# Performance work log

Measured on AMD Instinct MI355X. Metric: run time of the kernel, lower is better.

## Reference

```python
import jax, jax.numpy as jnp
import numpy as np

EPS = 1e-8


def setup_inputs() -> dict:
    key = jax.random.key(0)
    kx, kw = jax.random.split(key)
    B, T, D_IN, D_OUT = 2, 2048, 4096, 16384
    x = jax.random.normal(kx, (B, T, D_IN), dtype=jnp.float32)
    # kaiming-uniform-ish scale for a (D_OUT, D_IN) linear weight
    bound = float(np.sqrt(6.0 / D_IN))
    weight = jax.random.uniform(kw, (D_OUT, D_IN), dtype=jnp.float32,
                                minval=-bound, maxval=bound)
    return {"x": x, "weight": weight}


def reference(x, weight):
    # --- ternary weight quantization (STE; value identical in train/eval) ---
    scale_w = jnp.mean(jnp.abs(weight))                       # scalar absmean
    w_q = jnp.clip(jnp.round(weight / (scale_w + EPS)), -1.0, 1.0) * scale_w
    w_quant = weight + jax.lax.stop_gradient(w_q - weight)    # STE

    # --- per-token INT8 activation quantization ---
    gamma = jnp.max(jnp.abs(x), axis=-1, keepdims=True)       # (B, T, 1)
    x_quant = jnp.clip(jnp.round(127.0 * x / (gamma + EPS)), -128.0, 127.0)
    scale_x = gamma / 127.0                                   # (B, T, 1)

    # --- GEMM + dequant epilogue ---
    out = jnp.einsum("btd,od->bto", x_quant, w_quant)         # (B, T, D_OUT)
    return out * scale_x
```

## Files before the change

### kernel.cpp

```cpp
#include <hip/hip_runtime.h>


#define M_ROWS 4096
#define K_DIM  4096
#define N_DIM  16384
#define W_ELEMS (N_DIM * K_DIM)
#define EPSF 1e-8f

using i32x4 = __attribute__((ext_vector_type(4))) int;


__global__ void k_abs_partial(const float4* __restrict__ w4,
                              double* __restrict__ part) {
    const int tid = threadIdx.x;
    int idx = blockIdx.x * 256 + tid;
    double s = 0.0;
    #pragma unroll 4
    for (int it = 0; it < 32; ++it) {
        float4 v = w4[idx + it * (2048 * 256)];
        s += (double)fabsf(v.x) + (double)fabsf(v.y)
           + (double)fabsf(v.z) + (double)fabsf(v.w);
    }
    __shared__ double red[256];
    red[tid] = s;
    __syncthreads();
    for (int o = 128; o > 0; o >>= 1) {
        if (tid < o) red[tid] += red[tid + o];
        __syncthreads();
    }
    if (tid == 0) part[blockIdx.x] = red[0];
}

__global__ void k_abs_final(const double* __restrict__ part,
                            float* __restrict__ scales) {
    const int tid = threadIdx.x;
    double s = 0.0;
    #pragma unroll
    for (int k = 0; k < 8; ++k) s += part[tid + k * 256];
    __shared__ double red[256];
    red[tid] = s;
    __syncthreads();
    for (int o = 128; o > 0; o >>= 1) {
        if (tid < o) red[tid] += red[tid + o];
        __syncthreads();
    }
    if (tid == 0) {
        float sw = (float)(red[0] / (double)W_ELEMS);
        scales[0] = sw;
        scales[1] = sw + EPSF;
    }
}

__global__ void k_wquant(const float4* __restrict__ w4,
                         const float* __restrict__ scales,
                         char4* __restrict__ wq4) {
    const float seps = scales[1];
    int idx = blockIdx.x * 256 + threadIdx.x;
    const int stride = 8192 * 256;
    #pragma unroll
    for (int it = 0; it < 8; ++it) {
        int i = idx + it * stride;
        float4 v = w4[i];
        char4 q;
        q.x = (signed char)(int)fminf(fmaxf(rintf(v.x / seps), -1.0f), 1.0f);
        q.y = (signed char)(int)fminf(fmaxf(rintf(v.y / seps), -1.0f), 1.0f);
        q.z = (signed char)(int)fminf(fmaxf(rintf(v.z / seps), -1.0f), 1.0f);
        q.w = (signed char)(int)fminf(fmaxf(rintf(v.w / seps), -1.0f), 1.0f);
        wq4[i] = q;
    }
}

__global__ void k_xquant(const float4* __restrict__ x4,
                         char4* __restrict__ xq4,
                         float* __restrict__ sx) {
    const int row = blockIdx.x, tid = threadIdx.x;
    const float4* xr = x4 + (size_t)row * (K_DIM / 4);
    float4 v[4];
    float m = 0.0f;
    #pragma unroll
    for (int j = 0; j < 4; ++j) {
        v[j] = xr[tid + j * 256];
        m = fmaxf(m, fmaxf(fmaxf(fabsf(v[j].x), fabsf(v[j].y)),
                           fmaxf(fabsf(v[j].z), fabsf(v[j].w))));
    }
    __shared__ float red[256];
    red[tid] = m;
    __syncthreads();
    for (int o = 128; o > 0; o >>= 1) {
        if (tid < o) red[tid] = fmaxf(red[tid], red[tid + o]);
        __syncthreads();
    }
    const float gamma = red[0];
    const float ge = gamma + EPSF;
    char4* out = xq4 + (size_t)row * (K_DIM / 4);
    #pragma unroll
    for (int j = 0; j < 4; ++j) {
        char4 q;
        q.x = (signed char)(int)fminf(fmaxf(rintf(127.0f * v[j].x / ge), -128.0f), 127.0f);
        q.y = (signed char)(int)fminf(fmaxf(rintf(127.0f * v[j].y / ge), -128.0f), 127.0f);
        q.z = (signed char)(int)fminf(fmaxf(rintf(127.0f * v[j].z / ge), -128.0f), 127.0f);
        q.w = (signed char)(int)fminf(fmaxf(rintf(127.0f * v[j].w / ge), -128.0f), 127.0f);
        out[tid + j * 256] = q;
    }
    if (tid == 0) sx[row] = gamma / 127.0f;
}

__device__ __forceinline__ void gload16(const signed char* g, signed char* l) {
    __builtin_amdgcn_global_load_lds(
        (const __attribute__((address_space(1))) void*)g,
        (__attribute__((address_space(3))) void*)l, 16, 0, 0);
}

#define BAR()   __builtin_amdgcn_s_barrier()
#define LGKM0() asm volatile("s_waitcnt lgkmcnt(0)" ::: "memory")
#define VM6()   asm volatile("s_waitcnt vmcnt(6)" ::: "memory")
#define PRIO1() __builtin_amdgcn_s_setprio(1)
#define PRIO0() __builtin_amdgcn_s_setprio(0)

__global__ __launch_bounds__(512, 2)
void k_gemm8(const signed char* __restrict__ Aq,
             const signed char* __restrict__ Bq,
             const float* __restrict__ sx,
             const float* __restrict__ scales,
             float* __restrict__ C) {
    __shared__ __align__(16) signed char lds[131072];

    const int tid  = threadIdx.x;
    const int lane = tid & 63;
    const int wid  = tid >> 6;
    const int l15  = lane & 15;
    const int qg   = lane >> 4;
    const int swz  = l15 & 7;

    const int bid = blockIdx.x;
    const int wg  = (bid & 7) * 128 + (bid >> 3);
    const int gidx   = wg >> 9;
    const int within = wg & 511;
    const int pm = gidx * 8 + (within & 7);
    const int pn = within >> 3;

    const int wm = (wid >> 2) * 128;
    const int wn = (wid & 3) * 64;

    const int l3 = lane >> 3, l7 = lane & 7;
    const int lane_off = l3 * K_DIM + ((l7 ^ l3) << 4);
    const signed char* Asrc = Aq + (size_t)(pm * 256) * K_DIM + lane_off;
    const signed char* Bsrc = Bq + (size_t)(pn * 256) * K_DIM + lane_off;
    const int ar0 = wid * 8;
    const int br0 = (wid >> 2) * 64 + (wid & 3) * 8;

    auto stageA = [&](int buf, int mh, int kt) {
        const int r0 = mh * 64 + ar0;
        const signed char* s = Asrc + (size_t)r0 * K_DIM + kt * 128;
        signed char* d = lds + buf * 65536 + r0 * 128;
        gload16(s, d);
        gload16(s + (size_t)128 * K_DIM, d + 128 * 128);
    };
    auto stageB = [&](int buf, int nh, int kt) {
        const int r0 = nh * 32 + br0;
        const signed char* s = Bsrc + (size_t)r0 * K_DIM + kt * 128;
        signed char* d = lds + buf * 65536 + 32768 + r0 * 128;
        gload16(s, d);
        gload16(s + (size_t)128 * K_DIM, d + 128 * 128);
    };

    i32x4 acc[8][4];
    #pragma unroll
    for (int a = 0; a < 8; ++a)
        #pragma unroll
        for (int b = 0; b < 4; ++b)
            acc[a][b] = (i32x4){0, 0, 0, 0};

    i32x4 af[8], bf[4];
    auto ldA = [&](int buf, int mh) {
        const signed char* base = lds + buf * 65536;
        #pragma unroll
        for (int fm = 0; fm < 4; ++fm) {
            const int ro = (wm + mh * 64 + fm * 16 + l15) * 128;
            #pragma unroll
            for (int ks = 0; ks < 2; ++ks)
                af[fm * 2 + ks] = *(const i32x4*)(base + ro + (((ks * 4 + qg) ^ swz) << 4));
        }
    };
    auto ldB = [&](int buf, int nh) {
        const signed char* base = lds + buf * 65536 + 32768;
        #pragma unroll
        for (int fn = 0; fn < 2; ++fn) {
            const int ro = (wn + nh * 32 + fn * 16 + l15) * 128;
            #pragma unroll
            for (int ks = 0; ks < 2; ++ks)
                bf[fn * 2 + ks] = *(const i32x4*)(base + ro + (((ks * 4 + qg) ^ swz) << 4));
        }
    };
    auto mma = [&](int mh, int nh) {
        #pragma unroll
        for (int ks = 0; ks < 2; ++ks)
            #pragma unroll
            for (int fm = 0; fm < 4; ++fm)
                #pragma unroll
                for (int fn = 0; fn < 2; ++fn)
                    acc[mh * 4 + fm][nh * 2 + fn] = __builtin_amdgcn_mfma_i32_16x16x64_i8(
                        af[fm * 2 + ks], bf[fn * 2 + ks], acc[mh * 4 + fm][nh * 2 + fn], 0, 0, 0);
    };

    stageA(0, 0, 0); stageB(0, 1, 0); stageA(0, 1, 0); stageB(0, 0, 0);
    stageA(1, 0, 1); stageB(1, 1, 1); stageA(1, 1, 1);
    VM6();
    BAR();

    for (int t = 0; t < 16; ++t) {
        const int k1 = 2 * t + 1;
        const int k2 = (2 * t + 2) & 31;
        const int k3 = (2 * t + 3) & 31;

        ldA(0, 0); ldB(0, 0); stageB(1, 0, k1);
        BAR(); LGKM0(); PRIO1(); mma(0, 0); PRIO0(); BAR();
        ldB(0, 1); stageA(0, 0, k2);
        BAR(); LGKM0(); PRIO1(); mma(0, 1); PRIO0(); BAR();
        ldA(0, 1); stageB(0, 1, k2);
        BAR(); LGKM0(); PRIO1(); mma(1, 1); PRIO0(); BAR();
        ldB(0, 0); stageA(0, 1, k2);
        BAR(); LGKM0(); PRIO1(); mma(1, 0); PRIO0();
        VM6();
        BAR();
        ldA(1, 0); ldB(1, 0); stageB(0, 0, k2);
        BAR(); LGKM0(); PRIO1(); mma(0, 0); PRIO0(); BAR();
        ldB(1, 1); stageA(1, 0, k3);
        BAR(); LGKM0(); PRIO1(); mma(0, 1); PRIO0(); BAR();
        ldA(1, 1); stageB(1, 1, k3);
        BAR(); LGKM0(); PRIO1(); mma(1, 1); PRIO0(); BAR();
        ldB(1, 0); stageA(1, 1, k3);
        BAR(); LGKM0(); PRIO1(); mma(1, 0); PRIO0();
        VM6();
        BAR();
    }
    asm volatile("s_waitcnt vmcnt(0)" ::: "memory");

    const float sw = scales[0];
    const int gn0 = pn * 256 + wn + l15;
    const int rb  = (lane >> 4) * 4;
    #pragma unroll
    for (int mi = 0; mi < 8; ++mi) {
        const int rowoff = (mi >> 2) * 64 + (mi & 3) * 16;
        #pragma unroll
        for (int r = 0; r < 4; ++r) {
            const int gm = pm * 256 + wm + rowoff + rb + r;
            const float s = sx[gm] * sw;
            float* crow = C + (size_t)gm * N_DIM + gn0;
            #pragma unroll
            for (int ni = 0; ni < 4; ++ni)
                crow[(ni >> 1) * 32 + (ni & 1) * 16] = (float)acc[mi][ni][r] * s;
        }
    }
}

extern "C" void kernel_launch(void* const* d_in, const int* in_sizes, int n_in,
                              void* d_out, int out_size, void* d_ws, size_t ws_size,
                              hipStream_t stream) {
    const float* x = (const float*)d_in[0];
    const float* w = (const float*)d_in[1];
    float* out = (float*)d_out;
    char* ws = (char*)d_ws;

    float*  scales = (float*)(ws);
    double* part   = (double*)(ws + 1024);
    float*  sx     = (float*)(ws + 32 * 1024);
    signed char* xq = (signed char*)(ws + 64 * 1024);
    signed char* wq = xq + (size_t)M_ROWS * K_DIM;

    k_abs_partial<<<2048, 256, 0, stream>>>((const float4*)w, part);
    k_abs_final<<<1, 256, 0, stream>>>(part, scales);
    k_wquant<<<8192, 256, 0, stream>>>((const float4*)w, scales, (char4*)wq);
    k_xquant<<<M_ROWS, 256, 0, stream>>>((const float4*)x, (char4*)xq, sx);
    k_gemm8<<<(M_ROWS / 256) * (N_DIM / 256), 512, 0, stream>>>(xq, wq, sx, scales, out);
}
```

Baseline: 402.9 us.

## Double-buffer A/B register fragments and reorder LDS staging in GEMM main loop

Splits the A and B register fragments into two sets each, so all fragments for a k-tile are loaded from LDS in the first two phases and reused across the four MFMA quadrants. Global-to-LDS staging is reordered to match (B before A, a different staging order across phases). This cuts redundant LDS reads (B for nh=0 and A for mh=1 are no longer reloaded) and leaves two phases without LDS reads. It costs extra VGPRs, which may reduce occupancy or cause spills, and the changed staging order must stay consistent with the buffer hazards guarded by VM6 and the barriers.

```diff
diff --git a/kernel.cpp b/kernel.cpp
--- a/kernel.cpp
+++ b/kernel.cpp
@@ -8,7 +8,6 @@
 #define EPSF 1e-8f
 
 using i32x4 = __attribute__((ext_vector_type(4))) int;
-
 
 __global__ void k_abs_partial(const float4* __restrict__ w4,
                               double* __restrict__ part) {
@@ -171,8 +170,8 @@
         for (int b = 0; b < 4; ++b)
             acc[a][b] = (i32x4){0, 0, 0, 0};
 
-    i32x4 af[8], bf[4];
-    auto ldA = [&](int buf, int mh) {
+    i32x4 af0[8], af1[8], bf0[4], bf1[4];
+    auto ldA = [&](i32x4* af, int buf, int mh) {
         const signed char* base = lds + buf * 65536;
         #pragma unroll
         for (int fm = 0; fm < 4; ++fm) {
@@ -182,7 +181,7 @@
                 af[fm * 2 + ks] = *(const i32x4*)(base + ro + (((ks * 4 + qg) ^ swz) << 4));
         }
     };
-    auto ldB = [&](int buf, int nh) {
+    auto ldB = [&](i32x4* bf, int buf, int nh) {
         const signed char* base = lds + buf * 65536 + 32768;
         #pragma unroll
         for (int fn = 0; fn < 2; ++fn) {
@@ -192,7 +191,7 @@
                 bf[fn * 2 + ks] = *(const i32x4*)(base + ro + (((ks * 4 + qg) ^ swz) << 4));
         }
     };
-    auto mma = [&](int mh, int nh) {
+    auto mma = [&](const i32x4* af, const i32x4* bf, int mh, int nh) {
         #pragma unroll
         for (int ks = 0; ks < 2; ++ks)
             #pragma unroll
@@ -203,8 +202,8 @@
                         af[fm * 2 + ks], bf[fn * 2 + ks], acc[mh * 4 + fm][nh * 2 + fn], 0, 0, 0);
     };
 
-    stageA(0, 0, 0); stageB(0, 1, 0); stageA(0, 1, 0); stageB(0, 0, 0);
-    stageA(1, 0, 1); stageB(1, 1, 1); stageA(1, 1, 1);
+    stageB(0, 0, 0); stageB(0, 1, 0); stageA(0, 0, 0); stageA(0, 1, 0);
+    stageB(1, 0, 1); stageB(1, 1, 1); stageA(1, 0, 1);
     VM6();
     BAR();
 
@@ -213,24 +212,24 @@
         const int k2 = (2 * t + 2) & 31;
         const int k3 = (2 * t + 3) & 31;
 
-        ldA(0, 0); ldB(0, 0); stageB(1, 0, k1);
-        BAR(); LGKM0(); PRIO1(); mma(0, 0); PRIO0(); BAR();
-        ldB(0, 1); stageA(0, 0, k2);
-        BAR(); LGKM0(); PRIO1(); mma(0, 1); PRIO0(); BAR();
-        ldA(0, 1); stageB(0, 1, k2);
-        BAR(); LGKM0(); PRIO1(); mma(1, 1); PRIO0(); BAR();
-        ldB(0, 0); stageA(0, 1, k2);
-        BAR(); LGKM0(); PRIO1(); mma(1, 0); PRIO0();
+        ldB(bf0, 0, 0); ldA(af0, 0, 0); stageA(1, 1, k1);
+        BAR(); LGKM0(); PRIO1(); mma(af0, bf0, 0, 0); PRIO0(); BAR();
+        ldB(bf1, 0, 1); ldA(af1, 0, 1); stageB(0, 0, k2);
+        BAR(); LGKM0(); PRIO1(); mma(af0, bf1, 0, 1); PRIO0(); BAR();
+        stageB(0, 1, k2);
+        BAR(); LGKM0(); PRIO1(); mma(af1, bf1, 1, 1); PRIO0(); BAR();
+        stageA(0, 0, k2);
+        BAR(); LGKM0(); PRIO1(); mma(af1, bf0, 1, 0); PRIO0();
         VM6();
         BAR();
-        ldA(1, 0); ldB(1, 0); stageB(0, 0, k2);
-        BAR(); LGKM0(); PRIO1(); mma(0, 0); PRIO0(); BAR();
-        ldB(1, 1); stageA(1, 0, k3);
-        BAR(); LGKM0(); PRIO1(); mma(0, 1); PRIO0(); BAR();
-        ldA(1, 1); stageB(1, 1, k3);
-        BAR(); LGKM0(); PRIO1(); mma(1, 1); PRIO0(); BAR();
-        ldB(1, 0); stageA(1, 1, k3);
-        BAR(); LGKM0(); PRIO1(); mma(1, 0); PRIO0();
+        ldB(bf0, 1, 0); ldA(af0, 1, 0); stageA(0, 1, k2);
+        BAR(); LGKM0(); PRIO1(); mma(af0, bf0, 0, 0); PRIO0(); BAR();
+        ldB(bf1, 1, 1); ldA(af1, 1, 1); stageB(1, 0, k3);
+        BAR(); LGKM0(); PRIO1(); mma(af0, bf1, 0, 1); PRIO0(); BAR();
+        stageB(1, 1, k3);
+        BAR(); LGKM0(); PRIO1(); mma(af1, bf1, 1, 1); PRIO0(); BAR();
+        stageA(1, 0, k3);
+        BAR(); LGKM0(); PRIO1(); mma(af1, bf0, 1, 0); PRIO0();
         VM6();
         BAR();
     }
```

After: 543.1 us. 34.8% more time.
